# Optimization experiments

Measured on AMD Instinct MI355X. Metric: run time of the kernel, lower is better.

## Reference

```python
import jax, jax.numpy as jnp
import numpy as np

B, L, D_MODEL, N_HEADS = 8, 256, 2048, 8
D_HEAD = D_MODEL // N_HEADS  # 256 == L, required by DeltaRuleOperator broadcasting
ALPHA0, BETA0 = 0.1, 0.9      # delta_rule_strength, 1 - strength
LN_EPS = 1e-5


def setup_inputs() -> dict:
    k = jax.random.key(0)
    ks = jax.random.split(k, 8)
    s = 0.02
    return {
        "query": jax.random.normal(ks[0], (B, L, D_MODEL), jnp.float32),
        "key": jax.random.normal(ks[1], (B, L, D_MODEL), jnp.float32),
        "value": jax.random.normal(ks[2], (B, L, D_MODEL), jnp.float32),
        "Wq": jax.random.normal(ks[3], (D_MODEL, D_MODEL), jnp.float32) * s,
        "Wk": jax.random.normal(ks[4], (D_MODEL, D_MODEL), jnp.float32) * s,
        "Wv": jax.random.normal(ks[5], (D_MODEL, D_MODEL), jnp.float32) * s,
        "Wo": jax.random.normal(ks[6], (D_MODEL, D_MODEL), jnp.float32) * s,
        "bo": jnp.zeros((D_MODEL,), jnp.float32),
        "ln_g": jnp.ones((D_MODEL,), jnp.float32),
        "ln_b": jnp.zeros((D_MODEL,), jnp.float32),
        "alpha": jnp.asarray(ALPHA0, jnp.float32),
        "beta": jnp.asarray(BETA0, jnp.float32),
    }


def reference(query, key, value, Wq, Wk, Wv, Wo, bo, ln_g, ln_b, alpha, beta):
    Bs, Ls, D = query.shape
    H, Dh = N_HEADS, D // N_HEADS

    def proj(x, W):  # torch Linear: x @ W.T, split heads -> [B,H,L,Dh]
        return (x @ W.T).reshape(Bs, Ls, H, Dh).transpose(0, 2, 1, 3)

    Q = proj(query, Wq)
    K = proj(key, Wk)
    V = proj(value, Wv)

    # DeltaRuleOperator, applied sequentially per head (buffer mutates across heads)
    kv = jnp.einsum('bhld,bhmd->bhlm', K, V)  # [B,H,L,L] with L == Dh
    kv_heads = jnp.moveaxis(kv, 1, 0)          # [H,B,L,L]

    def cs_step(cs, kv_h):
        # cumulative_state = beta*cs + alpha*detach(mean(kv)); head uses pre-update cs
        new = beta * cs + alpha * jax.lax.stop_gradient(kv_h.mean(axis=(0, 1)))
        return new, cs

    _, cs_seq = jax.lax.scan(cs_step, jnp.zeros((Dh,), query.dtype), kv_heads)  # [H,Dh]
    cs_b = cs_seq[None, :, None, :]                       # [1,H,1,Dh]
    q_mod = Q * (cs_b + alpha * (kv - cs_b))              # delta-rule modulated queries

    # elu feature map
    phi = lambda x: jax.nn.elu(x) + 1.0
    pq, pk = phi(q_mod), phi(K)

    def time_major(x):  # [B,H,L,Dh] -> [L, B*H, Dh]
        return x.reshape(Bs * H, Ls, Dh).transpose(1, 0, 2)

    pq_t, pk_t, v_t = time_major(pq), time_major(pk), time_major(V)

    def step(carry, xs):
        S, Z = carry                        # S:[N,Dh,Dh], Z:[N,Dh]
        q_i, k_i, v_i = xs                  # each [N,Dh]
        S = S + k_i[:, :, None] * v_i[:, None, :]
        Z = Z + k_i
        num = jnp.einsum('nf,nfd->nd', q_i, S)
        den = jnp.maximum(jnp.sum(q_i * Z, axis=-1), 1e-8)
        return (S, Z), num / den[:, None]

    N = Bs * H
    S0 = jnp.zeros((N, Dh, Dh), query.dtype)
    Z0 = jnp.zeros((N, Dh), query.dtype)
    _, outs = jax.lax.scan(step, (S0, Z0), (pq_t, pk_t, v_t))  # [L,N,Dh]

    attn = outs.transpose(1, 0, 2).reshape(Bs, H, Ls, Dh)
    attn = attn.transpose(0, 2, 1, 3).reshape(Bs, Ls, D)       # concat heads

    o = attn @ Wo.T + bo                  # out_proj (dropout is identity in eval)
    x = query + o                          # residual + LayerNorm
    mu = x.mean(-1, keepdims=True)
    var = jnp.mean((x - mu) ** 2, axis=-1, keepdims=True)
    return (x - mu) / jnp.sqrt(var + LN_EPS) * ln_g + ln_b
```

## Files before the change

kernel.cpp:

```cpp
#include <hip/hip_runtime.h>
#include <hip/hip_bf16.h>

using u16 = unsigned short;

typedef __bf16 bf16x8 __attribute__((ext_vector_type(8)));
typedef float  f32x4  __attribute__((ext_vector_type(4)));

__device__ __forceinline__ float b2f(u16 u) {
  union { unsigned u; float f; } v; v.u = ((unsigned)u) << 16; return v.f;
}
__device__ __forceinline__ u16 f2b(float f) {
  union { float f; unsigned u; } v; v.f = f;
  unsigned r = v.u + 0x7fffu + ((v.u >> 16) & 1u);
  return (u16)(r >> 16);
}

__device__ __forceinline__ void gld_lds16(const void* g, void* l) {
  __builtin_amdgcn_global_load_lds(
      (__attribute__((address_space(1))) void*)(unsigned long long)(g),
      (__attribute__((address_space(3))) void*)(unsigned long long)(l),
      16, 0, 0);
}

template <int EPI, int BK>
__global__ __launch_bounds__(256) void gemm_bt(
    const u16* __restrict__ A, int lda, long sA1, long sA2,
    const u16* __restrict__ B, int ldb, long sB1, long sB2,
    void* __restrict__ Cv, int ldc, long sC1, long sC2,
    int K, int HDIV,
    const float* __restrict__ bias, const float* __restrict__ resid,
    float* __restrict__ partOut) {
  __shared__ __align__(16) u16 lds[2 * 128 * BK];
  __shared__ float denS[128];
  const int t = threadIdx.x;
  const int lane = t & 63;
  const int wave = t >> 6;
  const int wm = wave >> 1, wn = wave & 1;
  const int laneM = lane & 15, quad = lane >> 4;
  const int zb = blockIdx.z / HDIV, zh = blockIdx.z % HDIV;

  int bx = blockIdx.x, by = blockIdx.y;
  if (EPI == 2) { by = (bx >= 1) ? 1 : 0; bx = (bx == 2) ? 1 : 0; }
  const int kEnd = (EPI == 3) ? ((by + 1) * 128 < K ? (by + 1) * 128 : K) : K;

  const u16* Abase = A + zb * sA1 + zh * sA2 + (long)by * 128 * lda;
  const u16* Bbase = B + zb * sB1 + zh * sB2 + (long)bx * 128 * ldb;

  constexpr int STEPS = BK / 16;
  constexpr int RPS = 2048 / BK;
  constexpr int KK = BK / 32;
  const int sRow = (BK == 64) ? (t >> 3) : (t >> 2);
  const int sg = (BK == 64) ? (t & 7) : (t & 3);
  const int swz = (BK == 64) ? (sg ^ (sRow & 7)) : (sg ^ ((sRow >> 1) & 3));
  const int sc = swz * 8;

  f32x4 acc[4][4];
#pragma unroll
  for (int i = 0; i < 4; ++i)
#pragma unroll
    for (int j = 0; j < 4; ++j) acc[i][j] = (f32x4){0.f, 0.f, 0.f, 0.f};
  float dsum[4] = {0.f, 0.f, 0.f, 0.f};

  for (int k0 = 0; k0 < kEnd; k0 += BK) {
#pragma unroll
    for (int p = 0; p < STEPS; ++p)
      gld_lds16(Abase + (long)(p * RPS + sRow) * lda + k0 + sc,
                &lds[p * 2048 + t * 8]);
#pragma unroll
    for (int p = 0; p < STEPS; ++p)
      gld_lds16(Bbase + (long)(p * RPS + sRow) * ldb + k0 + sc,
                &lds[128 * BK + p * 2048 + t * 8]);
    __syncthreads();
    bf16x8 af[KK][4], bfv[KK][4];
#pragma unroll
    for (int kk = 0; kk < KK; ++kk) {
      int perm8;
      if (BK == 64) perm8 = ((kk * 4 + quad) ^ (laneM & 7)) * 8;
      else          perm8 = (quad ^ ((laneM >> 1) & 3)) * 8;
#pragma unroll
      for (int i = 0; i < 4; ++i) {
        af[kk][i] = *(const bf16x8*)&lds[(wm * 64 + i * 16 + laneM) * BK + perm8];
        bfv[kk][i] =
            *(const bf16x8*)&lds[128 * BK + (wn * 64 + i * 16 + laneM) * BK + perm8];
      }
    }
    if (EPI == 3) {
#pragma unroll
      for (int kk = 0; kk < KK; ++kk)
#pragma unroll
        for (int i = 0; i < 4; ++i) {
          union { bf16x8 v; u16 s[8]; } u; u.v = af[kk][i];
          float ds = 0.f;
#pragma unroll
          for (int e = 0; e < 8; ++e) ds += b2f(u.s[e]);
          dsum[i] += ds;
        }
    }
#pragma unroll
    for (int kk = 0; kk < KK; ++kk)
#pragma unroll
      for (int i = 0; i < 4; ++i)
#pragma unroll
        for (int j = 0; j < 4; ++j)
          acc[i][j] = __builtin_amdgcn_mfma_f32_16x16x32_bf16(
              af[kk][i], bfv[kk][j], acc[i][j], 0, 0, 0);
    __syncthreads();
  }

  if (EPI == 3) {
#pragma unroll
    for (int i = 0; i < 4; ++i) {
      float s = dsum[i];
      s += __shfl_xor(s, 16);
      s += __shfl_xor(s, 32);
      if (wn == 0 && quad == 0)
        denS[wm * 64 + i * 16 + laneM] = fmaxf(s, 1e-8f);
    }
    __syncthreads();
  }

  if (EPI == 1) {
#pragma unroll
    for (int j = 0; j < 4; ++j) {
      float s = 0.f;
#pragma unroll
      for (int i = 0; i < 4; ++i)
#pragma unroll
        for (int r = 0; r < 4; ++r) s += acc[i][j][r];
      s += __shfl_xor(s, 16);
      s += __shfl_xor(s, 32);
      if (quad == 0)
        atomicAdd(&partOut[zh * 256 + bx * 128 + wn * 64 + j * 16 + laneM], s);
    }
  }

  const long cOff = zb * sC1 + zh * sC2;
  const int colB = bx * 128 + wn * 64;
#pragma unroll
  for (int i = 0; i < 4; ++i) {
#pragma unroll
    for (int j = 0; j < 4; ++j) {
#pragma unroll
      for (int r = 0; r < 4; ++r) {
        const int lrow = wm * 64 + i * 16 + quad * 4 + r;
        const int row = by * 128 + lrow;
        const int col = colB + j * 16 + laneM;
        const long idx = cOff + (long)row * ldc + col;
        float v = acc[i][j][r];
        if (EPI == 0 || EPI == 1) {
          ((u16*)Cv)[idx] = f2b(v);
        } else if (EPI == 2) {
          ((u16*)Cv)[idx] = f2b(col <= row ? v : 0.0f);
        } else if (EPI == 3) {
          ((u16*)Cv)[idx] = f2b(v / denS[lrow]);
        } else {
          ((float*)Cv)[idx] =
              (zb == 0) ? v + bias[col] + resid[(long)row * ldc + col] : v;
        }
      }
    }
  }
}

__global__ __launch_bounds__(256) void convert7(
    const float* __restrict__ s0, const float* __restrict__ s1,
    const float* __restrict__ s2, const float* __restrict__ s3,
    const float* __restrict__ s4, const float* __restrict__ s5,
    const float* __restrict__ s6, u16* __restrict__ dst) {
  long idx = (long)blockIdx.x * 256 + threadIdx.x;
  int seg = (int)(idx >> 20);
  long off = (idx & 1048575) << 2;
  const float* s;
  switch (seg) {
    case 0: s = s0; break; case 1: s = s1; break; case 2: s = s2; break;
    case 3: s = s3; break; case 4: s = s4; break; case 5: s = s5; break;
    default: s = s6;
  }
  float4 v = *(const float4*)(s + off);
  ushort4 o;
  o.x = f2b(v.x); o.y = f2b(v.y); o.z = f2b(v.z); o.w = f2b(v.w);
  *(ushort4*)(dst + (long)seg * 4194304 + off) = o;
}

__global__ __launch_bounds__(256) void cs_kernel(
    const float* __restrict__ part, float* __restrict__ cs,
    const float* __restrict__ alphaP, const float* __restrict__ betaP) {
  int m = threadIdx.x;
  float alpha = *alphaP, beta = *betaP;
  float c = 0.f;
  for (int h = 0; h < 8; ++h) {
    cs[h * 256 + m] = c;
    c = beta * c + alpha * (part[h * 256 + m] * (1.0f / 2048.0f));
  }
}

__global__ __launch_bounds__(256) void pqpk_kernel(
    const u16* __restrict__ Qp, const u16* __restrict__ Kp,
    const u16* __restrict__ kv, const float* __restrict__ cs,
    const float* __restrict__ alphaP, u16* __restrict__ pq,
    u16* __restrict__ pk) {
  long idx = (long)blockIdx.x * 256 + threadIdx.x;
  int d = idx & 255, l = (int)((idx >> 8) & 255), h = (int)((idx >> 16) & 7),
      b = (int)(idx >> 19);
  float alpha = *alphaP;
  long pidx = ((long)(b * 256 + l)) * 2048 + h * 256 + d;
  float Qv = b2f(Qp[pidx]);
  float kvv = b2f(kv[idx]);
  float csv = cs[h * 256 + d];
  float qm = Qv * (csv + alpha * (kvv - csv));
  pq[idx] = f2b(qm > 0.f ? qm + 1.f : expf(qm));
  float Kv = b2f(Kp[pidx]);
  pk[idx] = f2b(Kv > 0.f ? Kv + 1.f : expf(Kv));
}

__global__ __launch_bounds__(256) void vtrans_kernel(const u16* __restrict__ Vp,
                                                     u16* __restrict__ Vt) {
  __shared__ u16 tile[32][33];
  int z = blockIdx.z, b = z >> 3, h = z & 7;
  int jT = blockIdx.x * 32, dT = blockIdx.y * 32;
  int tx = threadIdx.x, ty = threadIdx.y;
#pragma unroll
  for (int ii = 0; ii < 4; ++ii) {
    int j = jT + ty + ii * 8, d = dT + tx;
    tile[ty + ii * 8][tx] = Vp[(long)(b * 256 + j) * 2048 + h * 256 + d];
  }
  __syncthreads();
#pragma unroll
  for (int ii = 0; ii < 4; ++ii) {
    int d = dT + ty + ii * 8, j = jT + tx;
    Vt[(long)z * 65536 + d * 256 + j] = tile[tx][ty + ii * 8];
  }
}

__global__ __launch_bounds__(256) void ln_kernel(
    const float* __restrict__ x0, const float* __restrict__ x1,
    const float* __restrict__ g, const float* __restrict__ bb,
    float* __restrict__ out) {
  int row = blockIdx.x, t = threadIdx.x;
  const float4* xr0 = (const float4*)(x0 + (long)row * 2048);
  const float4* xr1 = (const float4*)(x1 + (long)row * 2048);
  float4 a0 = xr0[t], b0 = xr1[t], a1 = xr0[t + 256], b1 = xr1[t + 256];
  float4 v0, v1;
  v0.x = a0.x + b0.x; v0.y = a0.y + b0.y; v0.z = a0.z + b0.z; v0.w = a0.w + b0.w;
  v1.x = a1.x + b1.x; v1.y = a1.y + b1.y; v1.z = a1.z + b1.z; v1.w = a1.w + b1.w;
  float s = v0.x + v0.y + v0.z + v0.w + v1.x + v1.y + v1.z + v1.w;
  float ss = v0.x * v0.x + v0.y * v0.y + v0.z * v0.z + v0.w * v0.w +
             v1.x * v1.x + v1.y * v1.y + v1.z * v1.z + v1.w * v1.w;
  for (int o = 32; o; o >>= 1) { s += __shfl_xor(s, o); ss += __shfl_xor(ss, o); }
  __shared__ float a1s[4], a2s[4];
  int wave = t >> 6, lane = t & 63;
  if (lane == 0) { a1s[wave] = s; a2s[wave] = ss; }
  __syncthreads();
  s = a1s[0] + a1s[1] + a1s[2] + a1s[3];
  ss = a2s[0] + a2s[1] + a2s[2] + a2s[3];
  float mu = s * (1.f / 2048.f);
  float var = ss * (1.f / 2048.f) - mu * mu;
  float rstd = rsqrtf(var + 1e-5f);
  const float4* g4 = (const float4*)g;
  const float4* b4 = (const float4*)bb;
  float4* orow = (float4*)(out + (long)row * 2048);
  float4 gg = g4[t], bv = b4[t], r;
  r.x = (v0.x - mu) * rstd * gg.x + bv.x;
  r.y = (v0.y - mu) * rstd * gg.y + bv.y;
  r.z = (v0.z - mu) * rstd * gg.z + bv.z;
  r.w = (v0.w - mu) * rstd * gg.w + bv.w;
  orow[t] = r;
  gg = g4[t + 256]; bv = b4[t + 256];
  r.x = (v1.x - mu) * rstd * gg.x + bv.x;
  r.y = (v1.y - mu) * rstd * gg.y + bv.y;
  r.z = (v1.z - mu) * rstd * gg.z + bv.z;
  r.w = (v1.w - mu) * rstd * gg.w + bv.w;
  orow[t + 256] = r;
}

extern "C" void kernel_launch(void* const* d_in, const int* in_sizes, int n_in,
                              void* d_out, int out_size, void* d_ws,
                              size_t ws_size, hipStream_t stream) {
  const float* query = (const float*)d_in[0];
  const float* key = (const float*)d_in[1];
  const float* value = (const float*)d_in[2];
  const float* Wq = (const float*)d_in[3];
  const float* Wk = (const float*)d_in[4];
  const float* Wv = (const float*)d_in[5];
  const float* Wo = (const float*)d_in[6];
  const float* bo = (const float*)d_in[7];
  const float* ln_g = (const float*)d_in[8];
  const float* ln_b = (const float*)d_in[9];
  const float* alphaP = (const float*)d_in[10];
  const float* betaP = (const float*)d_in[11];

  char* ws = (char*)d_ws;
  const long SZ = 8388608;
  u16* qb = (u16*)(ws);
  u16* Wb = (u16*)(ws + 3 * SZ);
  u16* Qp = (u16*)(ws + 7 * SZ);
  u16* kvb = (u16*)(ws + 10 * SZ);
  u16* pq = (u16*)(ws + 12 * SZ);
  u16* pk = (u16*)(ws + 13 * SZ);
  u16* Vt = (u16*)(ws + 14 * SZ);
  u16* attnb = (u16*)(ws + 15 * SZ);
  u16* Ab = (u16*)(ws + 10 * SZ);
  float* x0 = (float*)(ws + 12 * SZ);
  float* x1 = (float*)(ws);
  float* part = (float*)(ws + 16 * SZ);
  float* cs = (float*)(ws + 16 * SZ + 16384);

  u16* Kp = Qp + 4194304;
  u16* Vp = Qp + 8388608;
  u16* Wob = Wb + 3 * 4194304;

  hipMemsetAsync(part, 0, 8 * 256 * sizeof(float), stream);

  convert7<<<28672, 256, 0, stream>>>(query, key, value, Wq, Wk, Wv, Wo, qb);

  gemm_bt<0, 32><<<dim3(16, 16, 3), 256, 0, stream>>>(
      qb, 2048, 4194304L, 0L, Wb, 2048, 4194304L, 0L, (void*)Qp, 2048,
      4194304L, 0L, 2048, 1, nullptr, nullptr, nullptr);

  gemm_bt<1, 64><<<dim3(2, 2, 64), 256, 0, stream>>>(
      Kp, 2048, 524288L, 256L, Vp, 2048, 524288L, 256L, (void*)kvb, 256,
      524288L, 65536L, 256, 8, nullptr, nullptr, part);

  cs_kernel<<<1, 256, 0, stream>>>(part, cs, alphaP, betaP);

  pqpk_kernel<<<16384, 256, 0, stream>>>(Qp, Kp, kvb, cs, alphaP, pq, pk);

  gemm_bt<2, 64><<<dim3(3, 1, 64), 256, 0, stream>>>(
      pq, 256, 524288L, 65536L, pk, 256, 524288L, 65536L, (void*)Ab, 256,
      524288L, 65536L, 256, 8, nullptr, nullptr, nullptr);

  vtrans_kernel<<<dim3(8, 8, 64), dim3(32, 8), 0, stream>>>(Vp, Vt);

  gemm_bt<3, 64><<<dim3(2, 2, 64), 256, 0, stream>>>(
      Ab, 256, 524288L, 65536L, Vt, 256, 524288L, 65536L, (void*)attnb, 2048,
      524288L, 256L, 256, 8, nullptr, nullptr, nullptr);

  gemm_bt<4, 32><<<dim3(16, 16, 2), 256, 0, stream>>>(
      attnb, 2048, 1024L, 0L, Wob, 2048, 1024L, 0L, (void*)x0, 2048,
      -25165824L, 0L, 1024, 1, bo, query, nullptr);

  ln_kernel<<<2048, 256, 0, stream>>>(x0, x1, ln_g, ln_b, (float*)d_out);
}
```

Measured before the change: 332.0 us.

## Split-K the QKV projection and fold partial-sum reduction into downstream kernels

The QKV projection GEMM is split along K into two halves, doubling the grid (16x16x6) to improve CU occupancy, and writes two bf16 partial outputs. The partials are summed in a new reduce_add for K, fused into the V transpose kernel for V, and folded into the pqpk elementwise kernel for Q. The cs scan kernel is removed by recomputing the cumulative state per thread, and pqpk is vectorized to 4 elements per thread. This adds extra partial-buffer traffic and an extra bf16 rounding of the partials, and the workspace layout is reshuffled.

```diff
diff --git a/kernel.cpp b/kernel.cpp
--- a/kernel.cpp
+++ b/kernel.cpp
@@ -182,39 +182,23 @@
   *(ushort4*)(dst + (long)seg * 4194304 + off) = o;
 }
 
-__global__ __launch_bounds__(256) void cs_kernel(
-    const float* __restrict__ part, float* __restrict__ cs,
-    const float* __restrict__ alphaP, const float* __restrict__ betaP) {
-  int m = threadIdx.x;
-  float alpha = *alphaP, beta = *betaP;
-  float c = 0.f;
-  for (int h = 0; h < 8; ++h) {
-    cs[h * 256 + m] = c;
-    c = beta * c + alpha * (part[h * 256 + m] * (1.0f / 2048.0f));
-  }
-}
-
-__global__ __launch_bounds__(256) void pqpk_kernel(
-    const u16* __restrict__ Qp, const u16* __restrict__ Kp,
-    const u16* __restrict__ kv, const float* __restrict__ cs,
-    const float* __restrict__ alphaP, u16* __restrict__ pq,
-    u16* __restrict__ pk) {
-  long idx = (long)blockIdx.x * 256 + threadIdx.x;
-  int d = idx & 255, l = (int)((idx >> 8) & 255), h = (int)((idx >> 16) & 7),
-      b = (int)(idx >> 19);
-  float alpha = *alphaP;
-  long pidx = ((long)(b * 256 + l)) * 2048 + h * 256 + d;
-  float Qv = b2f(Qp[pidx]);
-  float kvv = b2f(kv[idx]);
-  float csv = cs[h * 256 + d];
-  float qm = Qv * (csv + alpha * (kvv - csv));
-  pq[idx] = f2b(qm > 0.f ? qm + 1.f : expf(qm));
-  float Kv = b2f(Kp[pidx]);
-  pk[idx] = f2b(Kv > 0.f ? Kv + 1.f : expf(Kv));
-}
-
-__global__ __launch_bounds__(256) void vtrans_kernel(const u16* __restrict__ Vp,
-                                                     u16* __restrict__ Vt) {
+__global__ __launch_bounds__(256) void reduce_add(
+    const u16* __restrict__ a, const u16* __restrict__ b,
+    u16* __restrict__ o) {
+  long i = ((long)blockIdx.x * 256 + threadIdx.x) * 4;
+  ushort4 x = *(const ushort4*)&a[i];
+  ushort4 y = *(const ushort4*)&b[i];
+  ushort4 r;
+  r.x = f2b(b2f(x.x) + b2f(y.x));
+  r.y = f2b(b2f(x.y) + b2f(y.y));
+  r.z = f2b(b2f(x.z) + b2f(y.z));
+  r.w = f2b(b2f(x.w) + b2f(y.w));
+  *(ushort4*)&o[i] = r;
+}
+
+__global__ __launch_bounds__(256) void reduceV_kernel(
+    const u16* __restrict__ V0, const u16* __restrict__ V1,
+    u16* __restrict__ Vp, u16* __restrict__ Vt) {
   __shared__ u16 tile[32][33];
   int z = blockIdx.z, b = z >> 3, h = z & 7;
   int jT = blockIdx.x * 32, dT = blockIdx.y * 32;
@@ -222,7 +206,10 @@
 #pragma unroll
   for (int ii = 0; ii < 4; ++ii) {
     int j = jT + ty + ii * 8, d = dT + tx;
-    tile[ty + ii * 8][tx] = Vp[(long)(b * 256 + j) * 2048 + h * 256 + d];
+    long src = (long)(b * 256 + j) * 2048 + h * 256 + d;
+    u16 s = f2b(b2f(V0[src]) + b2f(V1[src]));
+    tile[ty + ii * 8][tx] = s;
+    Vp[src] = s;
   }
   __syncthreads();
 #pragma unroll
@@ -230,6 +217,44 @@
     int d = dT + ty + ii * 8, j = jT + tx;
     Vt[(long)z * 65536 + d * 256 + j] = tile[tx][ty + ii * 8];
   }
+}
+
+__global__ __launch_bounds__(256) void pqpk_kernel(
+    const u16* __restrict__ Q0, const u16* __restrict__ Q1,
+    const u16* __restrict__ Kp, const u16* __restrict__ kv,
+    const float* __restrict__ part, const float* __restrict__ alphaP,
+    const float* __restrict__ betaP, u16* __restrict__ pq,
+    u16* __restrict__ pk) {
+  long e = ((long)blockIdx.x * 256 + threadIdx.x) * 4;
+  int d = (int)(e & 255), l = (int)((e >> 8) & 255), h = (int)((e >> 16) & 7),
+      b = (int)(e >> 19);
+  float alpha = *alphaP, beta = *betaP;
+  float4 c = {0.f, 0.f, 0.f, 0.f};
+  for (int hh = 0; hh < h; ++hh) {
+    float4 p = *(const float4*)&part[hh * 256 + d];
+    c.x = beta * c.x + alpha * (p.x * (1.0f / 2048.0f));
+    c.y = beta * c.y + alpha * (p.y * (1.0f / 2048.0f));
+    c.z = beta * c.z + alpha * (p.z * (1.0f / 2048.0f));
+    c.w = beta * c.w + alpha * (p.w * (1.0f / 2048.0f));
+  }
+  long pidx = ((long)(b * 256 + l)) * 2048 + h * 256 + d;
+  ushort4 q0 = *(const ushort4*)&Q0[pidx];
+  ushort4 q1 = *(const ushort4*)&Q1[pidx];
+  ushort4 kk = *(const ushort4*)&Kp[pidx];
+  ushort4 kvv = *(const ushort4*)&kv[e];
+  ushort4 opq, opk;
+#define PQPK1(comp)                                                    \
+  {                                                                    \
+    float Qv = b2f(q0.comp) + b2f(q1.comp);                            \
+    float qm = Qv * (c.comp + alpha * (b2f(kvv.comp) - c.comp));       \
+    opq.comp = f2b(qm > 0.f ? qm + 1.f : expf(qm));                    \
+    float Kv = b2f(kk.comp);                                           \
+    opk.comp = f2b(Kv > 0.f ? Kv + 1.f : expf(Kv));                    \
+  }
+  PQPK1(x) PQPK1(y) PQPK1(z) PQPK1(w)
+#undef PQPK1
+  *(ushort4*)&pq[e] = opq;
+  *(ushort4*)&pk[e] = opk;
 }
 
 __global__ __launch_bounds__(256) void ln_kernel(
@@ -291,53 +316,59 @@
 
   char* ws = (char*)d_ws;
   const long SZ = 8388608;
+  const long SE = 4194304;
   u16* qb = (u16*)(ws);
   u16* Wb = (u16*)(ws + 3 * SZ);
-  u16* Qp = (u16*)(ws + 7 * SZ);
-  u16* kvb = (u16*)(ws + 10 * SZ);
-  u16* pq = (u16*)(ws + 12 * SZ);
-  u16* pk = (u16*)(ws + 13 * SZ);
-  u16* Vt = (u16*)(ws + 14 * SZ);
-  u16* attnb = (u16*)(ws + 15 * SZ);
-  u16* Ab = (u16*)(ws + 10 * SZ);
-  float* x0 = (float*)(ws + 12 * SZ);
-  float* x1 = (float*)(ws);
-  float* part = (float*)(ws + 16 * SZ);
-  float* cs = (float*)(ws + 16 * SZ + 16384);
-
-  u16* Kp = Qp + 4194304;
-  u16* Vp = Qp + 8388608;
-  u16* Wob = Wb + 3 * 4194304;
+  u16* P = (u16*)(ws + 7 * SZ);
+  u16* Q0 = P;
+  u16* K0 = P + 1 * SE;
+  u16* V0 = P + 2 * SE;
+  u16* Q1 = P + 3 * SE;
+  u16* K1 = P + 4 * SE;
+  u16* V1 = P + 5 * SE;
+  u16* Kp = (u16*)(ws + 13 * SZ);
+  u16* Vp = (u16*)(ws + 14 * SZ);
+  u16* Vt = (u16*)(ws);
+  u16* kvb = (u16*)(ws + 1 * SZ);
+  u16* Ab = kvb;
+  u16* pq = (u16*)(ws + 3 * SZ);
+  u16* pk = (u16*)(ws + 4 * SZ);
+  u16* attnb = (u16*)(ws + 5 * SZ);
+  u16* Wob = Wb + 3 * SE;
+  float* x0 = (float*)(ws + 8 * SZ);
+  float* x1 = (float*)(ws + 10 * SZ);
+  float* part = (float*)(ws + 15 * SZ);
 
   hipMemsetAsync(part, 0, 8 * 256 * sizeof(float), stream);
 
   convert7<<<28672, 256, 0, stream>>>(query, key, value, Wq, Wk, Wv, Wo, qb);
 
-  gemm_bt<0, 32><<<dim3(16, 16, 3), 256, 0, stream>>>(
-      qb, 2048, 4194304L, 0L, Wb, 2048, 4194304L, 0L, (void*)Qp, 2048,
-      4194304L, 0L, 2048, 1, nullptr, nullptr, nullptr);
+  gemm_bt<0, 32><<<dim3(16, 16, 6), 256, 0, stream>>>(
+      qb, 2048, 1024L, (long)SE, Wb, 2048, 1024L, (long)SE, (void*)P, 2048,
+      3 * SE, SE, 1024, 3, nullptr, nullptr, nullptr);
+
+  reduce_add<<<4096, 256, 0, stream>>>(K0, K1, Kp);
+
+  reduceV_kernel<<<dim3(8, 8, 64), dim3(32, 8), 0, stream>>>(V0, V1, Vp, Vt);
 
   gemm_bt<1, 64><<<dim3(2, 2, 64), 256, 0, stream>>>(
       Kp, 2048, 524288L, 256L, Vp, 2048, 524288L, 256L, (void*)kvb, 256,
       524288L, 65536L, 256, 8, nullptr, nullptr, part);
 
-  cs_kernel<<<1, 256, 0, stream>>>(part, cs, alphaP, betaP);
-
-  pqpk_kernel<<<16384, 256, 0, stream>>>(Qp, Kp, kvb, cs, alphaP, pq, pk);
+  pqpk_kernel<<<4096, 256, 0, stream>>>(Q0, Q1, Kp, kvb, part, alphaP, betaP,
+                                        pq, pk);
 
   gemm_bt<2, 64><<<dim3(3, 1, 64), 256, 0, stream>>>(
       pq, 256, 524288L, 65536L, pk, 256, 524288L, 65536L, (void*)Ab, 256,
       524288L, 65536L, 256, 8, nullptr, nullptr, nullptr);
 
-  vtrans_kernel<<<dim3(8, 8, 64), dim3(32, 8), 0, stream>>>(Vp, Vt);
-
   gemm_bt<3, 64><<<dim3(2, 2, 64), 256, 0, stream>>>(
       Ab, 256, 524288L, 65536L, Vt, 256, 524288L, 65536L, (void*)attnb, 2048,
       524288L, 256L, 256, 8, nullptr, nullptr, nullptr);
 
   gemm_bt<4, 32><<<dim3(16, 16, 2), 256, 0, stream>>>(
-      attnb, 2048, 1024L, 0L, Wob, 2048, 1024L, 0L, (void*)x0, 2048,
-      -25165824L, 0L, 1024, 1, bo, query, nullptr);
+      attnb, 2048, 1024L, 0L, Wob, 2048, 1024L, 0L, (void*)x0, 2048, (long)SE,
+      0L, 1024, 1, bo, query, nullptr);
 
   ln_kernel<<<2048, 256, 0, stream>>>(x0, x1, ln_g, ln_b, (float*)d_out);
 }
```

Measured after the change: 342.5 us. +3.2%, slower.

## Use 64-wide tiles for per-head GEMMs, fuse cumulative state into pqpk

Applied to the files above, without the earlier changes.

Adds a tile-size template parameter to the GEMM. The per-head kv, causal-score and attention-value GEMMs now use 64x64 tiles, giving 1024 blocks instead of 192–256. The causal score GEMM skips upper-triangle tiles with an early return. The single-block cs_kernel is removed: each pqpk thread recomputes the per-head cumulative state from the partial sums, and the pqpk kernel now handles four elements per thread with vector loads and stores. This aims to fill more compute units and drop one launch, at the cost of less reuse per tile and some repeated scan work in every thread.

```diff
diff --git a/kernel.cpp b/kernel.cpp
--- a/kernel.cpp
+++ b/kernel.cpp
@@ -22,7 +22,7 @@
       16, 0, 0);
 }
 
-template <int EPI, int BK>
+template <int EPI, int BK, int TM>
 __global__ __launch_bounds__(256) void gemm_bt(
     const u16* __restrict__ A, int lda, long sA1, long sA2,
     const u16* __restrict__ B, int ldb, long sB1, long sB2,
@@ -30,8 +30,13 @@
     int K, int HDIV,
     const float* __restrict__ bias, const float* __restrict__ resid,
     float* __restrict__ partOut) {
-  __shared__ __align__(16) u16 lds[2 * 128 * BK];
-  __shared__ float denS[128];
+  constexpr int WT = TM / 2;
+  constexpr int FR = WT / 16;
+  constexpr int KK = BK / 32;
+  constexpr int STEPS = TM * BK / 2048;
+  constexpr int RPS = 2048 / BK;
+  __shared__ __align__(16) u16 lds[2 * TM * BK];
+  __shared__ float denS[TM];
   const int t = threadIdx.x;
   const int lane = t & 63;
   const int wave = t >> 6;
@@ -39,27 +44,26 @@
   const int laneM = lane & 15, quad = lane >> 4;
   const int zb = blockIdx.z / HDIV, zh = blockIdx.z % HDIV;
 
-  int bx = blockIdx.x, by = blockIdx.y;
-  if (EPI == 2) { by = (bx >= 1) ? 1 : 0; bx = (bx == 2) ? 1 : 0; }
-  const int kEnd = (EPI == 3) ? ((by + 1) * 128 < K ? (by + 1) * 128 : K) : K;
-
-  const u16* Abase = A + zb * sA1 + zh * sA2 + (long)by * 128 * lda;
-  const u16* Bbase = B + zb * sB1 + zh * sB2 + (long)bx * 128 * ldb;
-
-  constexpr int STEPS = BK / 16;
-  constexpr int RPS = 2048 / BK;
-  constexpr int KK = BK / 32;
+  const int bx = blockIdx.x, by = blockIdx.y;
+  if (EPI == 2 && bx > by) return;
+  const int kEnd = (EPI == 3) ? ((by + 1) * TM < K ? (by + 1) * TM : K) : K;
+
+  const u16* Abase = A + zb * sA1 + zh * sA2 + (long)by * TM * lda;
+  const u16* Bbase = B + zb * sB1 + zh * sB2 + (long)bx * TM * ldb;
+
   const int sRow = (BK == 64) ? (t >> 3) : (t >> 2);
   const int sg = (BK == 64) ? (t & 7) : (t & 3);
   const int swz = (BK == 64) ? (sg ^ (sRow & 7)) : (sg ^ ((sRow >> 1) & 3));
   const int sc = swz * 8;
 
-  f32x4 acc[4][4];
-#pragma unroll
-  for (int i = 0; i < 4; ++i)
-#pragma unroll
-    for (int j = 0; j < 4; ++j) acc[i][j] = (f32x4){0.f, 0.f, 0.f, 0.f};
-  float dsum[4] = {0.f, 0.f, 0.f, 0.f};
+  f32x4 acc[FR][FR];
+#pragma unroll
+  for (int i = 0; i < FR; ++i)
+#pragma unroll
+    for (int j = 0; j < FR; ++j) acc[i][j] = (f32x4){0.f, 0.f, 0.f, 0.f};
+  float dsum[FR];
+#pragma unroll
+  for (int i = 0; i < FR; ++i) dsum[i] = 0.f;
 
   for (int k0 = 0; k0 < kEnd; k0 += BK) {
 #pragma unroll
@@ -69,26 +73,26 @@
 #pragma unroll
     for (int p = 0; p < STEPS; ++p)
       gld_lds16(Bbase + (long)(p * RPS + sRow) * ldb + k0 + sc,
-                &lds[128 * BK + p * 2048 + t * 8]);
+                &lds[TM * BK + p * 2048 + t * 8]);
     __syncthreads();
-    bf16x8 af[KK][4], bfv[KK][4];
+    bf16x8 af[KK][FR], bfv[KK][FR];
 #pragma unroll
     for (int kk = 0; kk < KK; ++kk) {
       int perm8;
       if (BK == 64) perm8 = ((kk * 4 + quad) ^ (laneM & 7)) * 8;
       else          perm8 = (quad ^ ((laneM >> 1) & 3)) * 8;
 #pragma unroll
-      for (int i = 0; i < 4; ++i) {
-        af[kk][i] = *(const bf16x8*)&lds[(wm * 64 + i * 16 + laneM) * BK + perm8];
+      for (int i = 0; i < FR; ++i) {
+        af[kk][i] = *(const bf16x8*)&lds[(wm * WT + i * 16 + laneM) * BK + perm8];
         bfv[kk][i] =
-            *(const bf16x8*)&lds[128 * BK + (wn * 64 + i * 16 + laneM) * BK + perm8];
+            *(const bf16x8*)&lds[TM * BK + (wn * WT + i * 16 + laneM) * BK + perm8];
       }
     }
     if (EPI == 3) {
 #pragma unroll
       for (int kk = 0; kk < KK; ++kk)
 #pragma unroll
-        for (int i = 0; i < 4; ++i) {
+        for (int i = 0; i < FR; ++i) {
           union { bf16x8 v; u16 s[8]; } u; u.v = af[kk][i];
           float ds = 0.f;
 #pragma unroll
@@ -99,9 +103,9 @@
 #pragma unroll
     for (int kk = 0; kk < KK; ++kk)
 #pragma unroll
-      for (int i = 0; i < 4; ++i)
-#pragma unroll
-        for (int j = 0; j < 4; ++j)
+      for (int i = 0; i < FR; ++i)
+#pragma unroll
+        for (int j = 0; j < FR; ++j)
           acc[i][j] = __builtin_amdgcn_mfma_f32_16x16x32_bf16(
               af[kk][i], bfv[kk][j], acc[i][j], 0, 0, 0);
     __syncthreads();
@@ -109,42 +113,41 @@
 
   if (EPI == 3) {
 #pragma unroll
-    for (int i = 0; i < 4; ++i) {
+    for (int i = 0; i < FR; ++i) {
       float s = dsum[i];
       s += __shfl_xor(s, 16);
       s += __shfl_xor(s, 32);
       if (wn == 0 && quad == 0)
-        denS[wm * 64 + i * 16 + laneM] = fmaxf(s, 1e-8f);
+        denS[wm * WT + i * 16 + laneM] = fmaxf(s, 1e-8f);
     }
     __syncthreads();
   }
 
   if (EPI == 1) {
 #pragma unroll
-    for (int j = 0; j < 4; ++j) {
+    for (int j = 0; j < FR; ++j) {
       float s = 0.f;
 #pragma unroll
-      for (int i = 0; i < 4; ++i)
+      for (int i = 0; i < FR; ++i)
 #pragma unroll
         for (int r = 0; r < 4; ++r) s += acc[i][j][r];
       s += __shfl_xor(s, 16);
       s += __shfl_xor(s, 32);
       if (quad == 0)
-        atomicAdd(&partOut[zh * 256 + bx * 128 + wn * 64 + j * 16 + laneM], s);
+        atomicAdd(&partOut[zh * 256 + bx * TM + wn * WT + j * 16 + laneM], s);
     }
   }
 
   const long cOff = zb * sC1 + zh * sC2;
-  const int colB = bx * 128 + wn * 64;
-#pragma unroll
-  for (int i = 0; i < 4; ++i) {
-#pragma unroll
-    for (int j = 0; j < 4; ++j) {
+#pragma unroll
+  for (int i = 0; i < FR; ++i) {
+#pragma unroll
+    for (int j = 0; j < FR; ++j) {
 #pragma unroll
       for (int r = 0; r < 4; ++r) {
-        const int lrow = wm * 64 + i * 16 + quad * 4 + r;
-        const int row = by * 128 + lrow;
-        const int col = colB + j * 16 + laneM;
+        const int lrow = wm * WT + i * 16 + quad * 4 + r;
+        const int row = by * TM + lrow;
+        const int col = bx * TM + wn * WT + j * 16 + laneM;
         const long idx = cOff + (long)row * ldc + col;
         float v = acc[i][j][r];
         if (EPI == 0 || EPI == 1) {
@@ -182,35 +185,40 @@
   *(ushort4*)(dst + (long)seg * 4194304 + off) = o;
 }
 
-__global__ __launch_bounds__(256) void cs_kernel(
-    const float* __restrict__ part, float* __restrict__ cs,
-    const float* __restrict__ alphaP, const float* __restrict__ betaP) {
-  int m = threadIdx.x;
-  float alpha = *alphaP, beta = *betaP;
-  float c = 0.f;
-  for (int h = 0; h < 8; ++h) {
-    cs[h * 256 + m] = c;
-    c = beta * c + alpha * (part[h * 256 + m] * (1.0f / 2048.0f));
-  }
-}
-
 __global__ __launch_bounds__(256) void pqpk_kernel(
     const u16* __restrict__ Qp, const u16* __restrict__ Kp,
-    const u16* __restrict__ kv, const float* __restrict__ cs,
-    const float* __restrict__ alphaP, u16* __restrict__ pq,
-    u16* __restrict__ pk) {
-  long idx = (long)blockIdx.x * 256 + threadIdx.x;
-  int d = idx & 255, l = (int)((idx >> 8) & 255), h = (int)((idx >> 16) & 7),
-      b = (int)(idx >> 19);
-  float alpha = *alphaP;
+    const u16* __restrict__ kv, const float* __restrict__ part,
+    const float* __restrict__ alphaP, const float* __restrict__ betaP,
+    u16* __restrict__ pq, u16* __restrict__ pk) {
+  long e = ((long)blockIdx.x * 256 + threadIdx.x) * 4;
+  int d = (int)(e & 255), l = (int)((e >> 8) & 255), h = (int)((e >> 16) & 7),
+      b = (int)(e >> 19);
+  float alpha = *alphaP, beta = *betaP;
+  float4 c = {0.f, 0.f, 0.f, 0.f};
+  for (int hh = 0; hh < h; ++hh) {
+    float4 p = *(const float4*)&part[hh * 256 + d];
+    c.x = beta * c.x + alpha * (p.x * (1.0f / 2048.0f));
+    c.y = beta * c.y + alpha * (p.y * (1.0f / 2048.0f));
+    c.z = beta * c.z + alpha * (p.z * (1.0f / 2048.0f));
+    c.w = beta * c.w + alpha * (p.w * (1.0f / 2048.0f));
+  }
   long pidx = ((long)(b * 256 + l)) * 2048 + h * 256 + d;
-  float Qv = b2f(Qp[pidx]);
-  float kvv = b2f(kv[idx]);
-  float csv = cs[h * 256 + d];
-  float qm = Qv * (csv + alpha * (kvv - csv));
-  pq[idx] = f2b(qm > 0.f ? qm + 1.f : expf(qm));
-  float Kv = b2f(Kp[pidx]);
-  pk[idx] = f2b(Kv > 0.f ? Kv + 1.f : expf(Kv));
+  ushort4 q0 = *(const ushort4*)&Qp[pidx];
+  ushort4 kk = *(const ushort4*)&Kp[pidx];
+  ushort4 kvv = *(const ushort4*)&kv[e];
+  ushort4 opq, opk;
+#define PQPK1(comp)                                                    \
+  {                                                                    \
+    float Qv = b2f(q0.comp);                                           \
+    float qm = Qv * (c.comp + alpha * (b2f(kvv.comp) - c.comp));       \
+    opq.comp = f2b(qm > 0.f ? qm + 1.f : expf(qm));                    \
+    float Kv = b2f(kk.comp);                                           \
+    opk.comp = f2b(Kv > 0.f ? Kv + 1.f : expf(Kv));                    \
+  }
+  PQPK1(x) PQPK1(y) PQPK1(z) PQPK1(w)
+#undef PQPK1
+  *(ushort4*)&pq[e] = opq;
+  *(ushort4*)&pk[e] = opk;
 }
 
 __global__ __launch_bounds__(256) void vtrans_kernel(const u16* __restrict__ Vp,
@@ -291,51 +299,49 @@
 
   char* ws = (char*)d_ws;
   const long SZ = 8388608;
+  const long SE = 4194304;
   u16* qb = (u16*)(ws);
   u16* Wb = (u16*)(ws + 3 * SZ);
   u16* Qp = (u16*)(ws + 7 * SZ);
+  u16* Kp = (u16*)(ws + 8 * SZ);
+  u16* Vp = (u16*)(ws + 9 * SZ);
   u16* kvb = (u16*)(ws + 10 * SZ);
+  u16* Ab = kvb;
   u16* pq = (u16*)(ws + 12 * SZ);
   u16* pk = (u16*)(ws + 13 * SZ);
   u16* Vt = (u16*)(ws + 14 * SZ);
   u16* attnb = (u16*)(ws + 15 * SZ);
-  u16* Ab = (u16*)(ws + 10 * SZ);
+  u16* Wob = Wb + 3 * SE;
   float* x0 = (float*)(ws + 12 * SZ);
   float* x1 = (float*)(ws);
   float* part = (float*)(ws + 16 * SZ);
-  float* cs = (float*)(ws + 16 * SZ + 16384);
-
-  u16* Kp = Qp + 4194304;
-  u16* Vp = Qp + 8388608;
-  u16* Wob = Wb + 3 * 4194304;
 
   hipMemsetAsync(part, 0, 8 * 256 * sizeof(float), stream);
 
   convert7<<<28672, 256, 0, stream>>>(query, key, value, Wq, Wk, Wv, Wo, qb);
 
-  gemm_bt<0, 32><<<dim3(16, 16, 3), 256, 0, stream>>>(
-      qb, 2048, 4194304L, 0L, Wb, 2048, 4194304L, 0L, (void*)Qp, 2048,
-      4194304L, 0L, 2048, 1, nullptr, nullptr, nullptr);
-
-  gemm_bt<1, 64><<<dim3(2, 2, 64), 256, 0, stream>>>(
+  gemm_bt<0, 32, 128><<<dim3(16, 16, 3), 256, 0, stream>>>(
+      qb, 2048, SE, 0L, Wb, 2048, SE, 0L, (void*)Qp, 2048, SE, 0L, 2048, 1,
+      nullptr, nullptr, nullptr);
+
+  gemm_bt<1, 64, 64><<<dim3(4, 4, 64), 256, 0, stream>>>(
       Kp, 2048, 524288L, 256L, Vp, 2048, 524288L, 256L, (void*)kvb, 256,
       524288L, 65536L, 256, 8, nullptr, nullptr, part);
 
-  cs_kernel<<<1, 256, 0, stream>>>(part, cs, alphaP, betaP);
-
-  pqpk_kernel<<<16384, 256, 0, stream>>>(Qp, Kp, kvb, cs, alphaP, pq, pk);
-
-  gemm_bt<2, 64><<<dim3(3, 1, 64), 256, 0, stream>>>(
+  pqpk_kernel<<<4096, 256, 0, stream>>>(Qp, Kp, kvb, part, alphaP, betaP, pq,
+                                        pk);
+
+  gemm_bt<2, 64, 64><<<dim3(4, 4, 64), 256, 0, stream>>>(
       pq, 256, 524288L, 65536L, pk, 256, 524288L, 65536L, (void*)Ab, 256,
       524288L, 65536L, 256, 8, nullptr, nullptr, nullptr);
 
   vtrans_kernel<<<dim3(8, 8, 64), dim3(32, 8), 0, stream>>>(Vp, Vt);
 
-  gemm_bt<3, 64><<<dim3(2, 2, 64), 256, 0, stream>>>(
+  gemm_bt<3, 64, 64><<<dim3(4, 4, 64), 256, 0, stream>>>(
       Ab, 256, 524288L, 65536L, Vt, 256, 524288L, 65536L, (void*)attnb, 2048,
       524288L, 256L, 256, 8, nullptr, nullptr, nullptr);
 
-  gemm_bt<4, 32><<<dim3(16, 16, 2), 256, 0, stream>>>(
+  gemm_bt<4, 32, 128><<<dim3(16, 16, 2), 256, 0, stream>>>(
       attnb, 2048, 1024L, 0L, Wob, 2048, 1024L, 0L, (void*)x0, 2048,
       -25165824L, 0L, 1024, 1, bo, query, nullptr);
 
```

New measurement: 332.4 us. Within noise of the previous version (+0.1%).
